# Performance work log

Hardware: AMD Instinct MI355X
Metric: run time of the kernel (lower is better)

## Reference

```python
import jax, jax.numpy as jnp
import numpy as np

ALPHA = 0.2  # LeakyReLU negative slope used throughout
NEG = -9e15


def _leaky(x, a=ALPHA):
    return jnp.where(x >= 0, x, a * x)


def _gat_layer(h, adj, W, a, concat):
    # h: [N, Fin], W: [Fin, Fout], a: [2*Fout, 1]
    Wh = h @ W                                   # [N, Fout]
    d = W.shape[-1]
    e = _leaky(Wh @ a[:d] + (Wh @ a[d:]).T)      # [N, N]
    att = jax.nn.softmax(jnp.where(adj > 0, e, NEG), axis=1)
    out = att @ Wh                               # [N, Fout]
    return jax.nn.elu(out) if concat else out


def setup_inputs() -> dict:
    key = jax.random.key(0)
    ks = jax.random.split(key, 24)
    N, F, H, D1, O1 = 4096, 512, 4, 256, 64
    x = jax.random.normal(ks[0], (N, F), dtype=jnp.float32)
    adj = jax.random.bernoulli(ks[1], 0.02, (N, N))
    adj = (adj | adj.T | jnp.eye(N, dtype=bool)).astype(jnp.float32)
    observation = jax.random.randint(ks[2], (1, N), 0, 2, dtype=jnp.int32)
    s_mat = jax.random.uniform(ks[3], (N, N), dtype=jnp.float32)
    theta = jax.random.uniform(ks[4], (1, F), dtype=jnp.float32)
    g = lambda k, s, sc: (jax.random.normal(k, s, dtype=jnp.float32) * sc)
    return {
        'x': x, 'adj': adj, 'observation': observation, 's_mat': s_mat,
        'theta': theta,
        'Wh0': g(ks[5], (H, F, D1), 0.05), 'ah0': g(ks[6], (H, 2 * D1, 1), 0.05),
        'Wh1': g(ks[7], (H, D1, D1), 0.05), 'ah1': g(ks[8], (H, 2 * D1, 1), 0.05),
        'Wo0': g(ks[9], (H * D1, O1), 0.05), 'ao0': g(ks[10], (2 * O1, 1), 0.05),
        'Wo1': g(ks[11], (O1, 1), 0.2), 'ao1': g(ks[12], (2, 1), 0.2),
        'dW': g(ks[13], (2, 10), 0.5), 'dW0': g(ks[14], (1, 10), 0.5),
        'dW1': g(ks[15], (10, 20), 0.5), 'dW01': g(ks[16], (1, 20), 0.5),
        'dW2': g(ks[17], (20, 10), 0.5), 'dW02': g(ks[18], (1, 10), 0.5),
        'dV': g(ks[19], (10, 1), 0.5), 'dV0': g(ks[20], (1, 1), 0.5),
    }


def reference(x, adj, observation, s_mat, theta, Wh0, ah0, Wh1, ah1,
              Wo0, ao0, Wo1, ao1, dW, dW0, dW1, dW01, dW2, dW02, dV, dV0):
    # mergeState: add theta to rows in the seed set (observation[0] == 1)
    seed = (observation[0] == 1).astype(x.dtype)[:, None]  # [N,1]
    h_in = x + seed * theta

    # multi-head 2-layer attention stacks (concat=True -> elu inside)
    def head(W0, a0, W1, a1):
        h = _gat_layer(h_in, adj, W0, a0, True)
        return _gat_layer(h, adj, W1, a1, True)

    hh = jax.vmap(head)(Wh0, ah0, Wh1, ah1)                 # [H, N, D1]
    hcat = jnp.transpose(hh, (1, 0, 2)).reshape(h_in.shape[0], -1)  # [N, H*D1]

    # output attention stack (concat=False), then elu (GAT.forward)
    h = _gat_layer(hcat, adj, Wo0, ao0, False)
    h = _gat_layer(h, adj, Wo1, ao1, False)
    h_ = jax.nn.elu(h)                                      # [N, 1]

    # GAT_degree v2: degreeNN over [h_, degree]
    d_v = s_mat.sum(axis=1, keepdims=True)                  # [N, 1]
    x_ = jnp.concatenate([h_, d_v], axis=1)                 # [N, 2]
    h0 = _leaky(x_ @ dW + dW0)
    h1 = _leaky(h0 @ dW1 + dW01)
    h2 = _leaky(h1 @ dW2 + dW02)
    return _leaky(h2 @ dV + dV0)                            # [N, 1]
```

## Files before the change

kernel.cpp:

```cpp
#include <hip/hip_runtime.h>
#include <hip/hip_bf16.h>
#include <hip/hip_fp16.h>
#include <math.h>

#define MAXDEG 512

typedef short v8s __attribute__((ext_vector_type(8)));
typedef float v4f __attribute__((ext_vector_type(4)));
typedef _Float16 h2 __attribute__((ext_vector_type(2)));

__device__ __forceinline__ float blockReduceSum(float v) {
    __shared__ float sh[8];
    int lane = threadIdx.x & 63, w = threadIdx.x >> 6;
    for (int o = 32; o > 0; o >>= 1) v += __shfl_down(v, o);
    __syncthreads();
    if (lane == 0) sh[w] = v;
    __syncthreads();
    if (w == 0) {
        int nw = (blockDim.x + 63) >> 6;
        v = (lane < nw) ? sh[lane] : 0.f;
        for (int o = 4; o > 0; o >>= 1) v += __shfl_down(v, o);
        if (lane == 0) sh[0] = v;
    }
    __syncthreads();
    return sh[0];
}

__device__ __forceinline__ float blockReduceMax(float v) {
    __shared__ float sh[8];
    int lane = threadIdx.x & 63, w = threadIdx.x >> 6;
    for (int o = 32; o > 0; o >>= 1) v = fmaxf(v, __shfl_down(v, o));
    __syncthreads();
    if (lane == 0) sh[w] = v;
    __syncthreads();
    if (w == 0) {
        int nw = (blockDim.x + 63) >> 6;
        v = (lane < nw) ? sh[lane] : -3.4e38f;
        for (int o = 4; o > 0; o >>= 1) v = fmaxf(v, __shfl_down(v, o));
        if (lane == 0) sh[0] = v;
    }
    __syncthreads();
    return sh[0];
}

__device__ __forceinline__ float leaky(float x) { return x >= 0.f ? x : 0.2f * x; }


__global__ void fused_pre(const float* __restrict__ adj, const float* __restrict__ s,
                          int* __restrict__ colIdx, int* __restrict__ deg,
                          float* __restrict__ dv,
                          const float* __restrict__ x, const int* __restrict__ obs,
                          const float* __restrict__ theta,
                          const float* __restrict__ Wh0, const float* __restrict__ Wh1,
                          const float* __restrict__ Wo0,
                          __half* __restrict__ hin, __half* __restrict__ Wh0t,
                          __half* __restrict__ Wh1t, __half* __restrict__ Wo0t,
                          float* __restrict__ elerZ, int elerN, int N) {
    const int tid = threadIdx.x;
    if (blockIdx.x < 4096) {
        int row = blockIdx.x;
        __shared__ int cnt;
        if (tid == 0) cnt = 0;
        __syncthreads();
        const float4* ar = (const float4*)(adj + (size_t)row * N);
        const float4* sr = (const float4*)(s + (size_t)row * N);
        int* outp = colIdx + (size_t)row * MAXDEG;
        float psum = 0.f;
        const int n4 = N >> 2;
        for (int j4 = tid; j4 < n4; j4 += blockDim.x) {
            float4 a4 = ar[j4];
            float4 s4 = sr[j4];
            psum += (s4.x + s4.y) + (s4.z + s4.w);
            int jb = j4 << 2;
            if (a4.x > 0.f) { int p = atomicAdd(&cnt, 1); if (p < MAXDEG) outp[p] = jb; }
            if (a4.y > 0.f) { int p = atomicAdd(&cnt, 1); if (p < MAXDEG) outp[p] = jb + 1; }
            if (a4.z > 0.f) { int p = atomicAdd(&cnt, 1); if (p < MAXDEG) outp[p] = jb + 2; }
            if (a4.w > 0.f) { int p = atomicAdd(&cnt, 1); if (p < MAXDEG) outp[p] = jb + 3; }
        }
        psum = blockReduceSum(psum);
        __syncthreads();
        if (tid == 0) {
            deg[row] = cnt < MAXDEG ? cnt : MAXDEG;
            dv[row] = psum;
        }
        return;
    }
    int bb = blockIdx.x - 4096;
    if (bb < 1024) {
        int i8 = bb * 256 + tid;
        int n = i8 >> 6;
        int f = (i8 & 63) * 8;
        float4 a = *(const float4*)(x + (size_t)i8 * 8);
        float4 b = *(const float4*)(x + (size_t)i8 * 8 + 4);
        if (obs[n] == 1) {
            float4 ta = *(const float4*)(theta + f);
            float4 tb = *(const float4*)(theta + f + 4);
            a.x += ta.x; a.y += ta.y; a.z += ta.z; a.w += ta.w;
            b.x += tb.x; b.y += tb.y; b.z += tb.z; b.w += tb.w;
        }
        __half hv[8];
        hv[0] = __float2half(a.x); hv[1] = __float2half(a.y);
        hv[2] = __float2half(a.z); hv[3] = __float2half(a.w);
        hv[4] = __float2half(b.x); hv[5] = __float2half(b.y);
        hv[6] = __float2half(b.z); hv[7] = __float2half(b.w);
        *(uint4*)(hin + (size_t)i8 * 8) = *(const uint4*)hv;
        return;
    }
    bb -= 1024;
    if (bb < 72) {
        int i = bb * 256 + tid;
        *(float4*)(elerZ + (size_t)i * 4) = make_float4(0.f, 0.f, 0.f, 0.f);
        return;
    }
    int t = bb - 72;
    const float* src;
    __half* dst;
    int srcStride, dstStride;
    if (t < 128) {
        int b = t >> 5, tt = t & 31, kt = tt >> 2, mt = tt & 3;
        src = Wh0 + b * 131072 + (kt * 64) * 256 + mt * 64;
        dst = Wh0t + b * 131072 + (mt * 64) * 512 + kt * 64;
        srcStride = 256; dstStride = 512;
    } else if (t < 192) {
        int u = t - 128;
        int b = u >> 4, tt = u & 15, kt = tt >> 2, mt = tt & 3;
        src = Wh1 + b * 65536 + (kt * 64) * 256 + mt * 64;
        dst = Wh1t + b * 65536 + (mt * 64) * 256 + kt * 64;
        srcStride = 256; dstStride = 256;
    } else {
        int kt = t - 192;
        src = Wo0 + (kt * 64) * 64;
        dst = Wo0t + kt * 64;
        srcStride = 64; dstStride = 1024;
    }
    __shared__ float tile[64][65];
    int rr = tid >> 4;
    int cc = (tid & 15) * 4;
    #pragma unroll
    for (int sI = 0; sI < 4; sI++) {
        float4 v = *(const float4*)(src + (size_t)(rr + sI * 16) * srcStride + cc);
        tile[rr + sI * 16][cc]     = v.x;
        tile[rr + sI * 16][cc + 1] = v.y;
        tile[rr + sI * 16][cc + 2] = v.z;
        tile[rr + sI * 16][cc + 3] = v.w;
    }
    __syncthreads();
    int mr = tid >> 2;
    int kc = (tid & 3) * 16;
    #pragma unroll
    for (int g = 0; g < 2; g++) {
        v8s v;
        #pragma unroll
        for (int e = 0; e < 8; e++)
            v[e] = (short)__half_as_ushort(__float2half(tile[kc + g * 8 + e][mr]));
        *(v8s*)(dst + (size_t)mr * dstStride + kc + g * 8) = v;
    }
}

__global__ __launch_bounds__(256) void gemm_mfma64x128(
    const __half* __restrict__ A, const __half* __restrict__ Bt,
    __half* __restrict__ C, int N, int K, int M,
    size_t sA, size_t sB, size_t sC,
    const float* __restrict__ aVec, size_t aStride,
    float* __restrict__ el, float* __restrict__ er) {
    int b = blockIdx.z;
    const unsigned short* Ag = (const unsigned short*)(A + (size_t)b * sA);
    const unsigned short* Bg = (const unsigned short*)(Bt + (size_t)b * sB);
    __half* Cg = C + (size_t)b * sC;
    const float* av = aVec + (size_t)b * aStride;

    __shared__ __align__(16) unsigned short As[64][72];
    __shared__ __align__(16) unsigned short Bs[128][72];

    const int tid = threadIdx.x;
    const int wave = tid >> 6, lane = tid & 63;
    const int wm = wave >> 1, wn = wave & 1;
    const int row0 = blockIdx.y * 64, col0 = blockIdx.x * 128;
    const int lr = tid >> 2;
    const int lo = (tid & 3) * 16;
    const int m = lane & 15, quad = lane >> 4;

    v4f acc[2][4];
    #pragma unroll
    for (int i = 0; i < 2; i++)
        #pragma unroll
        for (int c = 0; c < 4; c++) acc[i][c] = (v4f)(0.f);

    for (int k0 = 0; k0 < K; k0 += 64) {
        *(int4*)(&As[lr][lo]) =
            *(const int4*)(Ag + (size_t)(row0 + lr) * K + k0 + lo);
        *(int4*)(&As[lr][lo + 8]) =
            *(const int4*)(Ag + (size_t)(row0 + lr) * K + k0 + lo + 8);
        *(int4*)(&Bs[lr][lo]) =
            *(const int4*)(Bg + (size_t)(col0 + lr) * K + k0 + lo);
        *(int4*)(&Bs[lr][lo + 8]) =
            *(const int4*)(Bg + (size_t)(col0 + lr) * K + k0 + lo + 8);
        *(int4*)(&Bs[lr + 64][lo]) =
            *(const int4*)(Bg + (size_t)(col0 + 64 + lr) * K + k0 + lo);
        *(int4*)(&Bs[lr + 64][lo + 8]) =
            *(const int4*)(Bg + (size_t)(col0 + 64 + lr) * K + k0 + lo + 8);
        __syncthreads();
        #pragma unroll
        for (int ks = 0; ks < 2; ks++) {
            v8s af[2], bfv[4];
            #pragma unroll
            for (int i = 0; i < 2; i++)
                af[i] = *(const v8s*)(&As[wm * 32 + i * 16 + m][ks * 32 + quad * 8]);
            #pragma unroll
            for (int c = 0; c < 4; c++)
                bfv[c] = *(const v8s*)(&Bs[wn * 64 + c * 16 + m][ks * 32 + quad * 8]);
            #pragma unroll
            for (int i = 0; i < 2; i++)
                #pragma unroll
                for (int c = 0; c < 4; c++)
                    acc[i][c] = __builtin_amdgcn_mfma_f32_16x16x32_f16(
                        af[i], bfv[c], acc[i][c], 0, 0, 0);
        }
        __syncthreads();
    }
    #pragma unroll
    for (int i = 0; i < 2; i++)
        #pragma unroll
        for (int c = 0; c < 4; c++)
            #pragma unroll
            for (int r = 0; r < 4; r++) {
                int row = row0 + wm * 32 + i * 16 + quad * 4 + r;
                int col = col0 + wn * 64 + c * 16 + m;
                Cg[(size_t)row * M + col] = __float2half(acc[i][c][r]);
            }
    float ael[4], aer[4];
    #pragma unroll
    for (int c = 0; c < 4; c++) {
        ael[c] = av[col0 + wn * 64 + c * 16 + m];
        aer[c] = av[M + col0 + wn * 64 + c * 16 + m];
    }
    #pragma unroll
    for (int i = 0; i < 2; i++)
        #pragma unroll
        for (int r = 0; r < 4; r++) {
            float pel = 0.f, per_ = 0.f;
            #pragma unroll
            for (int c = 0; c < 4; c++) {
                pel += acc[i][c][r] * ael[c];
                per_ += acc[i][c][r] * aer[c];
            }
            #pragma unroll
            for (int off = 1; off < 16; off <<= 1) {
                pel += __shfl_xor(pel, off);
                per_ += __shfl_xor(per_, off);
            }
            if (m == 0) {
                int row = row0 + wm * 32 + i * 16 + quad * 4 + r;
                atomicAdd(&el[(size_t)b * N + row], pel);
                atomicAdd(&er[(size_t)b * N + row], per_);
            }
        }
}

__global__ __launch_bounds__(256) void gemm_mfma16(
    const __half* __restrict__ A, const __half* __restrict__ Bt,
    __half* __restrict__ C, int N, int K, int M,
    const float* __restrict__ aVec,
    float* __restrict__ el, float* __restrict__ er) {
    const unsigned short* Ag = (const unsigned short*)A;
    const unsigned short* Bg = (const unsigned short*)Bt;
    __half* Cg = C;
    const float* av = aVec;

    __shared__ __align__(16) unsigned short As[16][72];
    __shared__ __align__(16) unsigned short Bs[64][72];

    const int tid = threadIdx.x;
    const int wave = tid >> 6, lane = tid & 63;
    const int row0 = blockIdx.y * 16;
    const int m = lane & 15, quad = lane >> 4;

    v4f acc = (v4f)(0.f);

    for (int k0 = 0; k0 < K; k0 += 64) {
        if (tid < 128) {
            int ar = tid >> 3, ac = (tid & 7) * 8;
            *(int4*)(&As[ar][ac]) =
                *(const int4*)(Ag + (size_t)(row0 + ar) * K + k0 + ac);
        }
        {
            int br = tid >> 2, bc = (tid & 3) * 16;
            *(int4*)(&Bs[br][bc]) =
                *(const int4*)(Bg + (size_t)br * K + k0 + bc);
            *(int4*)(&Bs[br][bc + 8]) =
                *(const int4*)(Bg + (size_t)br * K + k0 + bc + 8);
        }
        __syncthreads();
        #pragma unroll
        for (int ks = 0; ks < 2; ks++) {
            v8s af = *(const v8s*)(&As[m][ks * 32 + quad * 8]);
            v8s bf = *(const v8s*)(&Bs[wave * 16 + m][ks * 32 + quad * 8]);
            acc = __builtin_amdgcn_mfma_f32_16x16x32_f16(af, bf, acc, 0, 0, 0);
        }
        __syncthreads();
    }
    #pragma unroll
    for (int r = 0; r < 4; r++) {
        int row = row0 + quad * 4 + r;
        int col = wave * 16 + m;
        Cg[(size_t)row * M + col] = __float2half(acc[r]);
    }
    float ael = av[wave * 16 + m];
    float aer = av[M + wave * 16 + m];
    #pragma unroll
    for (int r = 0; r < 4; r++) {
        float pel = acc[r] * ael;
        float per_ = acc[r] * aer;
        #pragma unroll
        for (int off = 1; off < 16; off <<= 1) {
            pel += __shfl_xor(pel, off);
            per_ += __shfl_xor(per_, off);
        }
        if (m == 0) {
            int row = row0 + quad * 4 + r;
            atomicAdd(&el[row], pel);
            atomicAdd(&er[row], per_);
        }
    }
}

template<int D, int ACT, int HEADS, int FUSE>
__global__ __launch_bounds__(128) void attn_vec(
    const __half* __restrict__ Wh, const float* __restrict__ el,
    const float* __restrict__ er, const int* __restrict__ colIdx,
    const int* __restrict__ deg, __half* __restrict__ out,
    int N, size_t sWh, size_t sOut, int outRowStride,
    const float* __restrict__ wo1, const float* __restrict__ ao1,
    float* __restrict__ o2wh, float* __restrict__ el4, float* __restrict__ er4) {
    constexpr int LPN = D / 8;
    constexpr int SUBS = 64 / LPN;
    constexpr int PER_WAVE = SUBS * 4;
    constexpr int STEP = PER_WAVE * 2;

    const int tid = threadIdx.x;
    const int wave = tid >> 6, lane = tid & 63;
    int b, row;
    if (HEADS == 4) {
        int xcd = blockIdx.x & 7;
        b = xcd >> 1;
        row = ((xcd & 1) << 11) + ((blockIdx.x >> 3) << 1) + wave;
    } else {
        b = 0;
        row = blockIdx.x * 2 + wave;
    }

    const __half* whb = Wh + (size_t)b * sWh;
    const float* erb = er + (size_t)b * N;
    const float eln = el[(size_t)b * N + row];
    const int dc = deg[row];
    const int dcp = (dc + STEP - 1) & ~(STEP - 1);
    const int* ci = colIdx + (size_t)row * MAXDEG;

    __shared__ __align__(16) float2 spc[2][MAXDEG];
    float2* sp = spc[wave];

    float sreg[8];
    int jreg[8];
    float mx = -3.4e38f;
    #pragma unroll
    for (int s8 = 0; s8 < 8; s8++) {
        int k = s8 * 64 + lane;
        if (k < dc) {
            int j = ci[k];
            float s = eln + erb[j];
            s = fmaxf(s, 0.2f * s);
            sreg[s8] = s;
            jreg[s8] = j * (D * 2);
            mx = fmaxf(mx, s);
        }
    }
    #pragma unroll
    for (int off = 1; off < 64; off <<= 1) mx = fmaxf(mx, __shfl_xor(mx, off));

    float l = 0.f;
    #pragma unroll
    for (int s8 = 0; s8 < 8; s8++) {
        int k = s8 * 64 + lane;
        if (k < dc) {
            float p = __expf(sreg[s8] - mx);
            l += p;
            unsigned int pu = __half_as_ushort(__float2half(p));
            sp[k] = make_float2(__int_as_float(pu | (pu << 16)),
                                __int_as_float(jreg[s8]));
        }
    }
    for (int k = dc + lane; k < dcp; k += 64)
        sp[k] = make_float2(__int_as_float(0), __int_as_float(0));
    #pragma unroll
    for (int off = 1; off < 64; off <<= 1) l += __shfl_xor(l, off);
    const float inv = 1.f / l;

    asm volatile("s_waitcnt lgkmcnt(0)" ::: "memory");

    const int sub = lane / LPN;
    const int dl = (lane % LPN) * 8;
    const char* wp = (const char*)(whb + dl);

    union HU { unsigned int u; h2 h; };
    union R4 { uint4 u; h2 h[4]; };

    h2 a0[4], a1[4], a2[4], a3[4];
    #pragma unroll
    for (int i = 0; i < 4; i++) {
        a0[i] = (h2)(_Float16)0; a1[i] = (h2)(_Float16)0;
        a2[i] = (h2)(_Float16)0; a3[i] = (h2)(_Float16)0;
    }

    for (int k = sub * 4; k < dcp; k += STEP) {
        float4 pA = *(const float4*)(&sp[k]);
        float4 pB = *(const float4*)(&sp[k + 2]);
        float4 pC = *(const float4*)(&sp[k + PER_WAVE]);
        float4 pD = *(const float4*)(&sp[k + PER_WAVE + 2]);
        R4 r0, r1, r2, r3, r4, r5, r6, r7;
        r0.u = *(const uint4*)(wp + __float_as_int(pA.y));
        r1.u = *(const uint4*)(wp + __float_as_int(pA.w));
        r2.u = *(const uint4*)(wp + __float_as_int(pB.y));
        r3.u = *(const uint4*)(wp + __float_as_int(pB.w));
        r4.u = *(const uint4*)(wp + __float_as_int(pC.y));
        r5.u = *(const uint4*)(wp + __float_as_int(pC.w));
        r6.u = *(const uint4*)(wp + __float_as_int(pD.y));
        r7.u = *(const uint4*)(wp + __float_as_int(pD.w));
        HU p0, p1, p2, p3, p4, p5, p6, p7;
        p0.u = __float_as_int(pA.x);
        p1.u = __float_as_int(pA.z);
        p2.u = __float_as_int(pB.x);
        p3.u = __float_as_int(pB.z);
        p4.u = __float_as_int(pC.x);
        p5.u = __float_as_int(pC.z);
        p6.u = __float_as_int(pD.x);
        p7.u = __float_as_int(pD.z);
        #pragma unroll
        for (int i = 0; i < 4; i++) {
            a0[i] += p0.h * r0.h[i];
            a1[i] += p2.h * r2.h[i];
            a2[i] += p4.h * r4.h[i];
            a3[i] += p6.h * r6.h[i];
        }
        #pragma unroll
        for (int i = 0; i < 4; i++) {
            a0[i] += p1.h * r1.h[i];
            a1[i] += p3.h * r3.h[i];
            a2[i] += p5.h * r5.h[i];
            a3[i] += p7.h * r7.h[i];
        }
    }
    #pragma unroll
    for (int i = 0; i < 4; i++) a0[i] += (a1[i] + (a2[i] + a3[i]));
    #pragma unroll
    for (int off = LPN; off < 64; off <<= 1)
        #pragma unroll
        for (int i = 0; i < 4; i++) {
            HU t, s;
            t.h = a0[i];
            s.u = __shfl_xor((int)t.u, off);
            a0[i] += s.h;
        }

    if (FUSE) {
        if (sub == 0) {
            float t = 0.f;
            #pragma unroll
            for (int i = 0; i < 4; i++) {
                t += (float)a0[i][0] * inv * wo1[dl + 2 * i];
                t += (float)a0[i][1] * inv * wo1[dl + 2 * i + 1];
            }
            #pragma unroll
            for (int off = 1; off < LPN; off <<= 1) t += __shfl_xor(t, off);
            if (lane == 0) {
                o2wh[row] = t;
                el4[row] = t * ao1[0];
                er4[row] = t * ao1[1];
            }
        }
        return;
    }
    if (sub == 0) {
        __half hv[8];
        #pragma unroll
        for (int i = 0; i < 4; i++) {
            float v0 = (float)a0[i][0] * inv;
            float v1 = (float)a0[i][1] * inv;
            if (ACT == 1) {
                v0 = (v0 > 0.f) ? v0 : expm1f(v0);
                v1 = (v1 > 0.f) ? v1 : expm1f(v1);
            }
            hv[2 * i]     = __float2half(v0);
            hv[2 * i + 1] = __float2half(v1);
        }
        *(uint4*)(out + (size_t)b * sOut + (size_t)row * outRowStride + dl) =
            *(const uint4*)hv;
    }
}

__global__ void attn_d1_deg(const float* __restrict__ o2wh, const float* __restrict__ el,
                            const float* __restrict__ er, const int* __restrict__ colIdx,
                            const int* __restrict__ deg, const float* __restrict__ dv,
                            const float* __restrict__ dW, const float* __restrict__ dW0,
                            const float* __restrict__ dW1, const float* __restrict__ dW01,
                            const float* __restrict__ dW2, const float* __restrict__ dW02,
                            const float* __restrict__ dV, const float* __restrict__ dV0,
                            float* __restrict__ out, int N) {
    int row = blockIdx.x, tid = threadIdx.x;
    const float eln = el[row];
    const int dc = deg[row];
    const int* ci = colIdx + (size_t)row * MAXDEG;
    __shared__ float sp[MAXDEG];
    __shared__ int sc[MAXDEG];
    float mx = -3.4e38f;
    for (int k = tid; k < dc; k += blockDim.x) {
        int j = ci[k];
        sc[k] = j;
        float s = eln + er[j];
        s = fmaxf(s, 0.2f * s);
        sp[k] = s;
        mx = fmaxf(mx, s);
    }
    mx = blockReduceMax(mx);
    float l = 0.f, acc = 0.f;
    for (int k = tid; k < dc; k += blockDim.x) {
        float p = __expf(sp[k] - mx);
        l += p;
        acc += p * o2wh[sc[k]];
    }
    l = blockReduceSum(l);
    acc = blockReduceSum(acc);
    if (tid == 0) {
        float h = acc / l;
        h = (h > 0.f) ? h : expm1f(h);
        float d = dv[row];
        float t0[10], t1[20], t2[10];
        #pragma unroll
        for (int i = 0; i < 10; i++)
            t0[i] = leaky(h * dW[i] + d * dW[10 + i] + dW0[i]);
        #pragma unroll
        for (int j = 0; j < 20; j++) {
            float s = dW01[j];
            #pragma unroll
            for (int i = 0; i < 10; i++) s += t0[i] * dW1[i * 20 + j];
            t1[j] = leaky(s);
        }
        #pragma unroll
        for (int j = 0; j < 10; j++) {
            float s = dW02[j];
            #pragma unroll
            for (int i = 0; i < 20; i++) s += t1[i] * dW2[i * 10 + j];
            t2[j] = leaky(s);
        }
        float o = dV0[0];
        #pragma unroll
        for (int i = 0; i < 10; i++) o += t2[i] * dV[i];
        out[row] = leaky(o);
    }
}

extern "C" void kernel_launch(void* const* d_in, const int* in_sizes, int n_in,
                              void* d_out, int out_size, void* d_ws, size_t ws_size,
                              hipStream_t stream) {
    const int N = 4096, F = 512, H = 4, D1 = 256, O1 = 64;
    const float* x     = (const float*)d_in[0];
    const float* adj   = (const float*)d_in[1];
    const int*   obs   = (const int*)  d_in[2];
    const float* s_mat = (const float*)d_in[3];
    const float* theta = (const float*)d_in[4];
    const float* Wh0   = (const float*)d_in[5];
    const float* ah0   = (const float*)d_in[6];
    const float* Wh1   = (const float*)d_in[7];
    const float* ah1   = (const float*)d_in[8];
    const float* Wo0   = (const float*)d_in[9];
    const float* ao0   = (const float*)d_in[10];
    const float* Wo1   = (const float*)d_in[11];
    const float* ao1   = (const float*)d_in[12];
    const float* dWp   = (const float*)d_in[13];
    const float* dW0p  = (const float*)d_in[14];
    const float* dW1p  = (const float*)d_in[15];
    const float* dW01p = (const float*)d_in[16];
    const float* dW2p  = (const float*)d_in[17];
    const float* dW02p = (const float*)d_in[18];
    const float* dVp   = (const float*)d_in[19];
    const float* dV0p  = (const float*)d_in[20];
    float* outp = (float*)d_out;

    char* ws = (char*)d_ws;
    auto alloc = [&](size_t bytes) {
        char* p = ws;
        ws += (bytes + 255) & ~(size_t)255;
        return p;
    };
    __half* hin  = (__half*)alloc((size_t)N * F * 2);
    __half* whA  = (__half*)alloc((size_t)H * N * D1 * 2);
    __half* hb   = (__half*)alloc((size_t)H * N * D1 * 2);
    __half* hcat = (__half*)alloc((size_t)N * H * D1 * 2);
    __half* o1Wh = (__half*)alloc((size_t)N * O1 * 2);
    float* o2Wh  = (float*)alloc((size_t)N * 4);
    __half* Wh0t = (__half*)alloc((size_t)H * F * D1 * 2);
    __half* Wh1t = (__half*)alloc((size_t)H * D1 * D1 * 2);
    __half* Wo0t = (__half*)alloc((size_t)H * D1 * O1 * 2);
    int elerN = 4 * H * N + 2 * N;
    float* elerZ = (float*)alloc((size_t)elerN * 4);
    float* el1 = elerZ;
    float* er1 = el1 + H * N;
    float* el2 = er1 + H * N;
    float* er2 = el2 + H * N;
    float* el3 = er2 + H * N;
    float* er3 = el3 + N;
    float* el4 = (float*)alloc((size_t)N * 4);
    float* er4 = (float*)alloc((size_t)N * 4);
    float* dv  = (float*)alloc((size_t)N * 4);
    int* colIdx = (int*)alloc((size_t)N * MAXDEG * 4);
    int* deg    = (int*)alloc((size_t)N * 4);

    {
        fused_pre<<<4096 + 1024 + 72 + 208, 256, 0, stream>>>(
            adj, s_mat, colIdx, deg, dv,
            x, obs, theta, Wh0, Wh1, Wo0, hin, Wh0t, Wh1t, Wo0t, elerZ, elerN, N);
    }

    gemm_mfma64x128<<<dim3(D1 / 128, N / 64, H), 256, 0, stream>>>(
        hin, Wh0t, whA, N, F, D1, 0, (size_t)D1 * F, (size_t)N * D1,
        ah0, (size_t)2 * D1, el1, er1);
    attn_vec<256, 1, 4, 0><<<(N * H) / 2, 128, 0, stream>>>(
        whA, el1, er1, colIdx, deg, hb,
        N, (size_t)N * D1, (size_t)N * D1, D1,
        nullptr, nullptr, nullptr, nullptr, nullptr);

    gemm_mfma64x128<<<dim3(D1 / 128, N / 64, H), 256, 0, stream>>>(
        hb, Wh1t, whA, N, D1, D1, (size_t)N * D1, (size_t)D1 * D1, (size_t)N * D1,
        ah1, (size_t)2 * D1, el2, er2);
    attn_vec<256, 1, 4, 0><<<(N * H) / 2, 128, 0, stream>>>(
        whA, el2, er2, colIdx, deg, hcat,
        N, (size_t)N * D1, (size_t)D1, H * D1,
        nullptr, nullptr, nullptr, nullptr, nullptr);

    gemm_mfma16<<<dim3(1, N / 16, 1), 256, 0, stream>>>(
        hcat, Wo0t, o1Wh, N, H * D1, O1,
        ao0, el3, er3);
    attn_vec<64, 0, 1, 1><<<N / 2, 128, 0, stream>>>(
        o1Wh, el3, er3, colIdx, deg, nullptr,
        N, 0, 0, O1,
        Wo1, ao1, o2Wh, el4, er4);

    attn_d1_deg<<<N, 256, 0, stream>>>(o2Wh, el4, er4, colIdx, deg, dv,
        dWp, dW0p, dW1p, dW01p, dW2p, dW02p, dVp, dV0p, outp, N);
}
```

Baseline: 377.3 us.

## Overlap adjacency CSR build with first-layer GEMM in one launch

The adjacency/s_mat scan that builds the column-index lists and row sums moves out of the preprocessing kernel into a combined kernel that also runs the first-layer attention GEMM for all heads as extra blocks. The memory-bound scan of two 64 MB matrices can then run concurrently with the compute-bound MFMA GEMM instead of before it. The GEMM blocks hardcode K, M and the per-head strides, and the combined kernel carries the larger shared-memory footprint of the GEMM, which may reduce how many scan blocks fit per CU.

```diff
diff --git a/kernel.cpp b/kernel.cpp
--- a/kernel.cpp
+++ b/kernel.cpp
@@ -46,46 +46,15 @@
 __device__ __forceinline__ float leaky(float x) { return x >= 0.f ? x : 0.2f * x; }
 
 
-__global__ void fused_pre(const float* __restrict__ adj, const float* __restrict__ s,
-                          int* __restrict__ colIdx, int* __restrict__ deg,
-                          float* __restrict__ dv,
-                          const float* __restrict__ x, const int* __restrict__ obs,
+__global__ void pre_small(const float* __restrict__ x, const int* __restrict__ obs,
                           const float* __restrict__ theta,
                           const float* __restrict__ Wh0, const float* __restrict__ Wh1,
                           const float* __restrict__ Wo0,
                           __half* __restrict__ hin, __half* __restrict__ Wh0t,
                           __half* __restrict__ Wh1t, __half* __restrict__ Wo0t,
-                          float* __restrict__ elerZ, int elerN, int N) {
+                          float* __restrict__ elerZ, int elerN) {
     const int tid = threadIdx.x;
-    if (blockIdx.x < 4096) {
-        int row = blockIdx.x;
-        __shared__ int cnt;
-        if (tid == 0) cnt = 0;
-        __syncthreads();
-        const float4* ar = (const float4*)(adj + (size_t)row * N);
-        const float4* sr = (const float4*)(s + (size_t)row * N);
-        int* outp = colIdx + (size_t)row * MAXDEG;
-        float psum = 0.f;
-        const int n4 = N >> 2;
-        for (int j4 = tid; j4 < n4; j4 += blockDim.x) {
-            float4 a4 = ar[j4];
-            float4 s4 = sr[j4];
-            psum += (s4.x + s4.y) + (s4.z + s4.w);
-            int jb = j4 << 2;
-            if (a4.x > 0.f) { int p = atomicAdd(&cnt, 1); if (p < MAXDEG) outp[p] = jb; }
-            if (a4.y > 0.f) { int p = atomicAdd(&cnt, 1); if (p < MAXDEG) outp[p] = jb + 1; }
-            if (a4.z > 0.f) { int p = atomicAdd(&cnt, 1); if (p < MAXDEG) outp[p] = jb + 2; }
-            if (a4.w > 0.f) { int p = atomicAdd(&cnt, 1); if (p < MAXDEG) outp[p] = jb + 3; }
-        }
-        psum = blockReduceSum(psum);
-        __syncthreads();
-        if (tid == 0) {
-            deg[row] = cnt < MAXDEG ? cnt : MAXDEG;
-            dv[row] = psum;
-        }
-        return;
-    }
-    int bb = blockIdx.x - 4096;
+    int bb = blockIdx.x;
     if (bb < 1024) {
         int i8 = bb * 256 + tid;
         int n = i8 >> 6;
@@ -155,6 +124,139 @@
             v[e] = (short)__half_as_ushort(__float2half(tile[kc + g * 8 + e][mr]));
         *(v8s*)(dst + (size_t)mr * dstStride + kc + g * 8) = v;
     }
+}
+
+__global__ __launch_bounds__(256) void gemm1_csr(
+    const __half* __restrict__ A, const __half* __restrict__ Bt,
+    __half* __restrict__ C,
+    const float* __restrict__ aVec, float* __restrict__ el, float* __restrict__ er,
+    const float* __restrict__ adj, const float* __restrict__ s,
+    int* __restrict__ colIdx, int* __restrict__ deg, float* __restrict__ dv,
+    int N) {
+    const int tid = threadIdx.x;
+    if (blockIdx.x < 4096) {
+        int row = blockIdx.x;
+        __shared__ int cnt;
+        if (tid == 0) cnt = 0;
+        __syncthreads();
+        const float4* ar = (const float4*)(adj + (size_t)row * N);
+        const float4* sr = (const float4*)(s + (size_t)row * N);
+        int* outp = colIdx + (size_t)row * MAXDEG;
+        float psum = 0.f;
+        const int n4 = N >> 2;
+        for (int j4 = tid; j4 < n4; j4 += 256) {
+            float4 a4 = ar[j4];
+            float4 s4 = sr[j4];
+            psum += (s4.x + s4.y) + (s4.z + s4.w);
+            int jb = j4 << 2;
+            if (a4.x > 0.f) { int p = atomicAdd(&cnt, 1); if (p < MAXDEG) outp[p] = jb; }
+            if (a4.y > 0.f) { int p = atomicAdd(&cnt, 1); if (p < MAXDEG) outp[p] = jb + 1; }
+            if (a4.z > 0.f) { int p = atomicAdd(&cnt, 1); if (p < MAXDEG) outp[p] = jb + 2; }
+            if (a4.w > 0.f) { int p = atomicAdd(&cnt, 1); if (p < MAXDEG) outp[p] = jb + 3; }
+        }
+        psum = blockReduceSum(psum);
+        __syncthreads();
+        if (tid == 0) {
+            deg[row] = cnt < MAXDEG ? cnt : MAXDEG;
+            dv[row] = psum;
+        }
+        return;
+    }
+    const int g = blockIdx.x - 4096;
+    const int bx = g & 1, by = (g >> 1) & 63, bz = g >> 7;
+    const int K = 512, M = 256;
+    const unsigned short* Ag = (const unsigned short*)A;
+    const unsigned short* Bg = (const unsigned short*)Bt + (size_t)bz * 131072;
+    __half* Cg = C + (size_t)bz * 4096 * 256;
+    const float* av = aVec + (size_t)bz * 512;
+    float* elb = el + (size_t)bz * 4096;
+    float* erb = er + (size_t)bz * 4096;
+
+    __shared__ __align__(16) unsigned short As[64][72];
+    __shared__ __align__(16) unsigned short Bs[128][72];
+
+    const int wave = tid >> 6, lane = tid & 63;
+    const int wm = wave >> 1, wn = wave & 1;
+    const int row0 = by * 64, col0 = bx * 128;
+    const int lr = tid >> 2;
+    const int lo = (tid & 3) * 16;
+    const int m = lane & 15, quad = lane >> 4;
+
+    v4f acc[2][4];
+    #pragma unroll
+    for (int i = 0; i < 2; i++)
+        #pragma unroll
+        for (int c = 0; c < 4; c++) acc[i][c] = (v4f)(0.f);
+
+    for (int k0 = 0; k0 < K; k0 += 64) {
+        *(int4*)(&As[lr][lo]) =
+            *(const int4*)(Ag + (size_t)(row0 + lr) * K + k0 + lo);
+        *(int4*)(&As[lr][lo + 8]) =
+            *(const int4*)(Ag + (size_t)(row0 + lr) * K + k0 + lo + 8);
+        *(int4*)(&Bs[lr][lo]) =
+            *(const int4*)(Bg + (size_t)(col0 + lr) * K + k0 + lo);
+        *(int4*)(&Bs[lr][lo + 8]) =
+            *(const int4*)(Bg + (size_t)(col0 + lr) * K + k0 + lo + 8);
+        *(int4*)(&Bs[lr + 64][lo]) =
+            *(const int4*)(Bg + (size_t)(col0 + 64 + lr) * K + k0 + lo);
+        *(int4*)(&Bs[lr + 64][lo + 8]) =
+            *(const int4*)(Bg + (size_t)(col0 + 64 + lr) * K + k0 + lo + 8);
+        __syncthreads();
+        #pragma unroll
+        for (int ks = 0; ks < 2; ks++) {
+            v8s af[2], bfv[4];
+            #pragma unroll
+            for (int i = 0; i < 2; i++)
+                af[i] = *(const v8s*)(&As[wm * 32 + i * 16 + m][ks * 32 + quad * 8]);
+            #pragma unroll
+            for (int c = 0; c < 4; c++)
+                bfv[c] = *(const v8s*)(&Bs[wn * 64 + c * 16 + m][ks * 32 + quad * 8]);
+            #pragma unroll
+            for (int i = 0; i < 2; i++)
+                #pragma unroll
+                for (int c = 0; c < 4; c++)
+                    acc[i][c] = __builtin_amdgcn_mfma_f32_16x16x32_f16(
+                        af[i], bfv[c], acc[i][c], 0, 0, 0);
+        }
+        __syncthreads();
+    }
+    #pragma unroll
+    for (int i = 0; i < 2; i++)
+        #pragma unroll
+        for (int c = 0; c < 4; c++)
+            #pragma unroll
+            for (int r = 0; r < 4; r++) {
+                int row = row0 + wm * 32 + i * 16 + quad * 4 + r;
+                int col = col0 + wn * 64 + c * 16 + m;
+                Cg[(size_t)row * M + col] = __float2half(acc[i][c][r]);
+            }
+    float ael[4], aer[4];
+    #pragma unroll
+    for (int c = 0; c < 4; c++) {
+        ael[c] = av[col0 + wn * 64 + c * 16 + m];
+        aer[c] = av[M + col0 + wn * 64 + c * 16 + m];
+    }
+    #pragma unroll
+    for (int i = 0; i < 2; i++)
+        #pragma unroll
+        for (int r = 0; r < 4; r++) {
+            float pel = 0.f, per_ = 0.f;
+            #pragma unroll
+            for (int c = 0; c < 4; c++) {
+                pel += acc[i][c][r] * ael[c];
+                per_ += acc[i][c][r] * aer[c];
+            }
+            #pragma unroll
+            for (int off = 1; off < 16; off <<= 1) {
+                pel += __shfl_xor(pel, off);
+                per_ += __shfl_xor(per_, off);
+            }
+            if (m == 0) {
+                int row = row0 + wm * 32 + i * 16 + quad * 4 + r;
+                atomicAdd(&elb[row], pel);
+                atomicAdd(&erb[row], per_);
+            }
+        }
 }
 
 __global__ __launch_bounds__(256) void gemm_mfma64x128(
@@ -614,15 +716,12 @@
     int* colIdx = (int*)alloc((size_t)N * MAXDEG * 4);
     int* deg    = (int*)alloc((size_t)N * 4);
 
-    {
-        fused_pre<<<4096 + 1024 + 72 + 208, 256, 0, stream>>>(
-            adj, s_mat, colIdx, deg, dv,
-            x, obs, theta, Wh0, Wh1, Wo0, hin, Wh0t, Wh1t, Wo0t, elerZ, elerN, N);
-    }
-
-    gemm_mfma64x128<<<dim3(D1 / 128, N / 64, H), 256, 0, stream>>>(
-        hin, Wh0t, whA, N, F, D1, 0, (size_t)D1 * F, (size_t)N * D1,
-        ah0, (size_t)2 * D1, el1, er1);
+    pre_small<<<1024 + 72 + 208, 256, 0, stream>>>(
+        x, obs, theta, Wh0, Wh1, Wo0, hin, Wh0t, Wh1t, Wo0t, elerZ, elerN);
+
+    gemm1_csr<<<4096 + 512, 256, 0, stream>>>(
+        hin, Wh0t, whA, ah0, el1, er1,
+        adj, s_mat, colIdx, deg, dv, N);
     attn_vec<256, 1, 4, 0><<<(N * H) / 2, 128, 0, stream>>>(
         whA, el1, er1, colIdx, deg, hb,
         N, (size_t)N * D1, (size_t)N * D1, D1,
```

Result: slower. 385.4 us (+2.1%).
